# Kernel optimization log

Measured on AMD Instinct MI355X. Metric: run time of the kernel, lower is better.

Reference implementation:

```python
import jax, jax.numpy as jnp
import numpy as np

B, T, H, W, C = 2, 8, 20, 36, 512
NH = 4
HD = C // NH
WS = (5, 9)
EXP = (2, 4)              # window_size // 2
KP = (5, 9)               # focal unfold kernel for level k=0
PADP = (2, 4)
T2T_K, T2T_S, T2T_P = (7, 7), (3, 3), (3, 3)
FFN_HD = 1960
NWH, NWW = H // WS[0], W // WS[1]   # 4, 4
WAREA = WS[0] * WS[1]               # 45


def _valid_ind_rolled():
    wh, ww = WS
    eh, ew = EXP
    m = np.ones((4, wh, ww), np.float32)
    m[0, :wh - eh, :ww - ew] = 0   # tl
    m[1, :wh - eh, ew:] = 0        # tr
    m[2, eh:, :ww - ew] = 0        # bl
    m[3, eh:, ew:] = 0             # br
    return jnp.asarray(np.nonzero(m.reshape(-1))[0])

VALID_ROLLED = _valid_ind_rolled()  # (120,)


def unfold(x, k, s, p):
    # x: (N, Cc, Hh, Ww) -> (N, Cc*kh*kw, L); matches torch.nn.Unfold layout (c slowest).
    N, Cc, Hh, Ww = x.shape
    kh, kw = k; sh, sw = s; ph, pw = p
    xp = jnp.pad(x, ((0, 0), (0, 0), (ph, ph), (pw, pw)))
    oh = (Hh + 2 * ph - kh) // sh + 1
    ow = (Ww + 2 * pw - kw) // sw + 1
    cols = [xp[:, :, i:i + oh * sh:sh, j:j + ow * sw:sw]
            for i in range(kh) for j in range(kw)]
    patches = jnp.stack(cols, axis=2)            # (N, Cc, kh*kw, oh, ow)
    return patches.reshape(N, Cc * kh * kw, oh * ow)


def fold(patches, out_hw, k, s, p):
    # inverse of unfold (overlap-add), matches torch F.fold.
    N = patches.shape[0]
    kh, kw = k; sh, sw = s; ph, pw = p
    Hh, Ww = out_hw
    oh = (Hh + 2 * ph - kh) // sh + 1
    ow = (Ww + 2 * pw - kw) // sw + 1
    Cc = patches.shape[1] // (kh * kw)
    pr = patches.reshape(N, Cc, kh, kw, oh, ow)
    out = jnp.zeros((N, Cc, Hh + 2 * ph, Ww + 2 * pw), patches.dtype)
    for i in range(kh):
        for j in range(kw):
            out = out.at[:, :, i:i + oh * sh:sh, j:j + ow * sw:sw].add(pr[:, :, i, j])
    return out[:, :, ph:ph + Hh, pw:pw + Ww]


def layer_norm(x, g, b):
    mu = jnp.mean(x, -1, keepdims=True)
    var = jnp.var(x, -1, keepdims=True)
    return (x - mu) * jax.lax.rsqrt(var + 1e-5) * g + b


def win_part(x):
    # (B,T,H,W,C) -> (B*nW, T*wh*ww, C)
    b = x.shape[0]
    x = x.reshape(b, T, NWH, WS[0], NWW, WS[1], C)
    return x.transpose(0, 2, 4, 1, 3, 5, 6).reshape(-1, T * WAREA, C)


def to_heads(w):
    return w.reshape(-1, T, WAREA, NH, HD).transpose(0, 3, 1, 2, 4).reshape(-1, NH, T * WAREA, HD)


def block_forward(x, g1, be1, wqkv, bqkv, wproj, bproj, wpool, bpool, g2, be2, w1, bf1, w2, bf2, out_h, out_w):
    shortcut = x
    xn = layer_norm(x, g1, be1)

    # ---- coarser (pooled) focal level, k=0 (focal_level=2) ----
    wnr = xn.reshape(B, T, NWH, WS[0], NWW, WS[1], C).transpose(0, 2, 4, 1, 3, 5, 6)
    wnr = wnr.reshape(B, NWH, NWW, T, WAREA, C)
    pooled = jnp.einsum('bhwtnc,n->bhwtc', wnr, wpool) + bpool   # (B,NWH,NWW,T,C)

    # ---- window attention ----
    qkv = xn @ wqkv + bqkv                                       # (B,T,H,W,3C)
    q, k, v = jnp.split(qkv, 3, axis=-1)
    qw = to_heads(win_part(q)) * (HD ** -0.5)
    kw_, vw = to_heads(win_part(k)), to_heads(win_part(v))

    def rolled(t):
        parts = []
        for sh, sw in ((-EXP[0], -EXP[1]), (-EXP[0], EXP[1]), (EXP[0], -EXP[1]), (EXP[0], EXP[1])):
            r = jnp.roll(t, (sh, sw), axis=(2, 3))
            parts.append(win_part(r).reshape(-1, T, WAREA, NH, HD))
        cat = jnp.concatenate(parts, axis=2)                     # (B*nW, T, 4*warea, NH, HD)
        cat = jnp.take(cat.transpose(0, 3, 1, 2, 4), VALID_ROLLED, axis=3)
        return cat.reshape(-1, NH, T * VALID_ROLLED.shape[0], HD)

    k_rolled = jnp.concatenate([kw_, rolled(k)], axis=2)         # (B*nW, NH, T*165, HD)
    v_rolled = jnp.concatenate([vw, rolled(v)], axis=2)

    # pooled keys/values via focal unfold
    xp = pooled.transpose(0, 3, 1, 2, 4)                          # (B,T,NWH,NWW,C)
    qkv_p = xp @ wqkv + bqkv
    kp, vp = qkv_p[..., C:2 * C], qkv_p[..., 2 * C:]

    def unfold_kv(t):
        t = t.transpose(0, 1, 4, 2, 3).reshape(B * T, C, NWH, NWW)
        u = unfold(t, KP, (1, 1), PADP)                           # (B*T, C*45, L)
        L = u.shape[-1]
        u = u.reshape(B, T, C, KP[0], KP[1], L).transpose(0, 5, 1, 3, 4, 2)
        u = u.reshape(B * L, T, KP[0] * KP[1], NH, HD).transpose(0, 3, 1, 2, 4)
        return u.reshape(B * L, NH, T * KP[0] * KP[1], HD)

    k_all = jnp.concatenate([k_rolled, unfold_kv(kp)], axis=2)
    v_all = jnp.concatenate([v_rolled, unfold_kv(vp)], axis=2)

    attn = jnp.einsum('wnqd,wnkd->wnqk', qw, k_all)               # (B*nW, NH, T*45, N)

    # validity mask for pooled context (zero-padded unfold positions -> -100)
    ones = jnp.ones((T, 1, NWH, NWW), x.dtype)
    um = unfold(ones, KP, (1, 1), PADP)                           # (T, 45, L)
    L = um.shape[-1]
    mvals = jnp.where(um.reshape(T, KP[0] * KP[1], L).transpose(2, 0, 1).reshape(L, -1) == 0,
                      jnp.asarray(-100.0, x.dtype), jnp.asarray(0.0, x.dtype))
    n_rolled = k_rolled.shape[2]
    mask_cols = jnp.concatenate([jnp.zeros((L, n_rolled), x.dtype), mvals], axis=1)
    attn = attn + jnp.tile(mask_cols, (B, 1))[:, None, None, :]

    attn = jax.nn.softmax(attn, axis=-1)
    out = jnp.einsum('wnqk,wnkd->wnqd', attn, v_all)
    out = out.transpose(0, 2, 1, 3).reshape(-1, T * WAREA, C) @ wproj + bproj

    # window reverse + residual
    out = out.reshape(B, NWH, NWW, T, WS[0], WS[1], C)
    out = out.transpose(0, 3, 1, 4, 2, 5, 6).reshape(B, T, H, W, C)
    x = shortcut + out

    # ---- FusionFeedForward (fold/unfold re-normalized MLP) ----
    y = layer_norm(x, g2, be2).reshape(B, T * H * W, C)
    h = y @ w1 + bf1                                              # (B, n, 1960)
    nvec = ((out_h + 2 * T2T_P[0] - T2T_K[0]) // T2T_S[0] + 1) * \
           ((out_w + 2 * T2T_P[1] - T2T_K[1]) // T2T_S[1] + 1)
    bt = (B * T * H * W) // nvec
    norm_p = jnp.ones((bt, T2T_K[0] * T2T_K[1], nvec), x.dtype)
    norm_f = fold(norm_p, (out_h, out_w), T2T_K, T2T_S, T2T_P)    # (bt,1,out_h,out_w)
    h_f = fold(h.reshape(bt, nvec, FFN_HD).transpose(0, 2, 1), (out_h, out_w), T2T_K, T2T_S, T2T_P)
    h = unfold(h_f / norm_f, T2T_K, T2T_S, T2T_P).transpose(0, 2, 1).reshape(B, T * H * W, FFN_HD)
    h = jax.nn.gelu(h, approximate=False) @ w2 + bf2
    return x + h.reshape(B, T, H, W, C)


def setup_inputs() -> dict:
    key = jax.random.key(0)
    ks = jax.random.split(key, 8)
    s = 0.02
    return dict(
        x=jax.random.normal(ks[0], (B, T, H, W, C), jnp.float32),
        g1=jnp.ones((C,), jnp.float32),
        be1=jnp.zeros((C,), jnp.float32),
        wqkv=jax.random.normal(ks[1], (C, 3 * C), jnp.float32) * s,
        bqkv=jnp.zeros((3 * C,), jnp.float32),
        wproj=jax.random.normal(ks[2], (C, C), jnp.float32) * s,
        bproj=jnp.zeros((C,), jnp.float32),
        wpool=jnp.full((WAREA,), 1.0 / WAREA, jnp.float32),
        bpool=jnp.zeros((1,), jnp.float32),
        g2=jnp.ones((C,), jnp.float32),
        be2=jnp.zeros((C,), jnp.float32),
        w1=jax.random.normal(ks[3], (C, FFN_HD), jnp.float32) * s,
        bf1=jnp.zeros((FFN_HD,), jnp.float32),
        w2=jax.random.normal(ks[4], (FFN_HD, C), jnp.float32) * s,
        bf2=jnp.zeros((C,), jnp.float32),
        out_h=60,
        out_w=108,
    )


def reference(x, g1, be1, wqkv, bqkv, wproj, bproj, wpool, bpool, g2, be2, w1, bf1, w2, bf2, out_h, out_w):
    return block_forward(x, g1, be1, wqkv, bqkv, wproj, bproj, wpool, bpool,
                         g2, be2, w1, bf1, w2, bf2, out_h, out_w)
```

## Files before the change

kernel.cpp:

```cpp
#include <hip/hip_runtime.h>
#include <hip/hip_bf16.h>
#include <math.h>

typedef __hip_bfloat16 bf16;
typedef __attribute__((ext_vector_type(8))) short bf16x8;
typedef __attribute__((ext_vector_type(4))) float f32x4;

#define DEVI __device__ __forceinline__

#define C_ 512
#define NH_ 4
#define NTOK 11520
#define NKEY 1680
#define NRK 120
#define FFN_ 1960
#define POOLED_FLAG 0x40000000

DEVI float bfu(unsigned u) { return __uint_as_float(u << 16); }
DEVI void stw(bf16* p, float v) { *p = __float2bfloat16(v); }
DEVI unsigned short f2bs(float f) { bf16 h = __float2bfloat16(f); return *(unsigned short*)&h; }
DEVI unsigned pk2(float a, float b) {
  return (unsigned)f2bs(a) | ((unsigned)f2bs(b) << 16);
}
DEVI float ldwr(const void* p, size_t i, int dt) {
  return dt ? ((const float*)p)[i] : __bfloat162float(((const bf16*)p)[i]);
}

DEVI void gload_lds16(const void* g, void* l) {
  __builtin_amdgcn_global_load_lds(
      (const __attribute__((address_space(1))) void*)g,
      (__attribute__((address_space(3))) void*)l, 16, 0, 0);
}

__global__ void k_detect(const void* __restrict__ g1, int* __restrict__ flag) {
  if (threadIdx.x == 0) {
    const unsigned short* p = (const unsigned short*)g1;
    *flag = (p[0] == 0x3F80u) ? 0 : 1;
  }
}

__global__ void k_prep(int* __restrict__ table) {
  if (threadIdx.x == 0) {
    int cnt = 0;
    for (int p = 0; p < 4; p++)
      for (int wi = 0; wi < 5; wi++)
        for (int wj = 0; wj < 9; wj++) {
          bool invalid;
          if (p == 0)      invalid = (wi < 3) && (wj < 5);
          else if (p == 1) invalid = (wi < 3) && (wj >= 4);
          else if (p == 2) invalid = (wi >= 2) && (wj < 5);
          else             invalid = (wi >= 2) && (wj >= 4);
          if (!invalid) table[cnt++] = p * 45 + wi * 9 + wj;
        }
  }
}

__global__ void k_ksrc(const int* __restrict__ vtab, int* __restrict__ ksrc) {
  int idx = blockIdx.x * 256 + threadIdx.x;
  if (idx >= 32 * NKEY) return;
  int w = idx / NKEY, j = idx % NKEY;
  int b = w >> 4, nh = (w >> 2) & 3, nw = w & 3;
  int val;
  if (j < 360) {
    int t = j / 45, pos = j % 45, wi = pos / 9, wj2 = pos % 9;
    val = ((b * 8 + t) * 20 + nh * 5 + wi) * 36 + nw * 9 + wj2;
  } else if (j < 1320) {
    int jj = j - 360;
    int t = jj / 120, r = jj % 120;
    int id = vtab[r];
    int p = id / 45, pos = id % 45, wi = pos / 9, wj2 = pos % 9;
    int sh = (p < 2) ? -2 : 2;
    int sw = (p & 1) ? 4 : -4;
    int hh = nh * 5 + wi - sh;
    if (hh < 0) hh += 20; else if (hh >= 20) hh -= 20;
    int ww2 = nw * 9 + wj2 - sw;
    if (ww2 < 0) ww2 += 36; else if (ww2 >= 36) ww2 -= 36;
    val = ((b * 8 + t) * 20 + hh) * 36 + ww2;
  } else {
    int jj = j - 1320;
    int t = jj / 45, kidx = jj % 45, ki = kidx / 9, kj = kidx % 9;
    int snh = nh + ki - 2, snw = nw + kj - 4;
    if (snh < 0 || snh >= 4 || snw < 0 || snw >= 4) val = -1;
    else val = POOLED_FLAG | ((b * 8 + t) * 16 + snh * 4 + snw);
  }
  ksrc[idx] = val;
}

__global__ void k_wcvt_all(const int* __restrict__ dflag,
                           const void* __restrict__ w0, const void* __restrict__ w1i,
                           const void* __restrict__ w2i, const void* __restrict__ w3i,
                           bf16* __restrict__ o0, bf16* __restrict__ o1,
                           bf16* __restrict__ o2, bf16* __restrict__ o3) {
  __shared__ unsigned short tile[64][65];
  const int dt = *dflag;
  int bid = blockIdx.x;
  const void* in; bf16* out; int K, N, nn;
  if (bid < 192)      { in = w0;  out = o0; K = 512;  N = 1536; nn = 24; }
  else if (bid < 256) { in = w1i; out = o1; K = 512;  N = 512;  nn = 8;  bid -= 192; }
  else if (bid < 512) { in = w2i; out = o2; K = 512;  N = 1960; nn = 32; bid -= 256; }
  else                { in = w3i; out = o3; K = 1960; N = 512;  nn = 8;  bid -= 512; }
  int tn = bid % nn, tk = bid / nn;
  int n0 = tn * 64, k0 = tk * 64;
  int cr = threadIdx.x >> 6;
  int cc = threadIdx.x & 63;
#pragma unroll
  for (int p = 0; p < 16; p++) {
    int kr = p * 4 + cr;
    float v = 0.f;
    if (k0 + kr < K && n0 + cc < N)
      v = ldwr(in, (size_t)(k0 + kr) * N + n0 + cc, dt);
    tile[kr][cc] = f2bs(v);
  }
  __syncthreads();
#pragma unroll
  for (int p = 0; p < 16; p++) {
    int nr = p * 4 + cr;
    int k = k0 + cc;
    if (k < K) {
      unsigned short u = tile[cc][nr];
      out[(size_t)(n0 + nr) * K + k] = *(bf16*)&u;
    }
  }
}

__global__ void k_bcvt_all(const int* __restrict__ dflag,
                           const void* __restrict__ b0, const void* __restrict__ b1,
                           const void* __restrict__ b2, const void* __restrict__ b3,
                           float* __restrict__ o0, float* __restrict__ o1,
                           float* __restrict__ o2, float* __restrict__ o3) {
  const int dt = *dflag;
  int i = blockIdx.x * 256 + threadIdx.x;
  if (i < 1536)      o0[i] = ldwr(b0, i, dt);
  else if (i < 2048) o1[i - 1536] = ldwr(b1, i - 1536, dt);
  else if (i < 4008) o2[i - 2048] = ldwr(b2, i - 2048, dt);
  else if (i < 4520) o3[i - 4008] = ldwr(b3, i - 4008, dt);
}

__global__ void k_ln(const int* __restrict__ dflag, int xmode,
                     const void* __restrict__ xin, const void* __restrict__ g,
                     const void* __restrict__ be, bf16* __restrict__ out) {
  const int dt = *dflag;
  const int xf32 = xmode | dt;
  const int tok = blockIdx.x;
  const int tid = threadIdx.x;
  const size_t base = (size_t)tok * C_;
  float v0 = ldwr(xin, base + tid, xf32);
  float v1 = ldwr(xin, base + tid + 256, xf32);
  float s = v0 + v1, ss = v0 * v0 + v1 * v1;
#pragma unroll
  for (int o = 32; o; o >>= 1) { s += __shfl_xor(s, o); ss += __shfl_xor(ss, o); }
  __shared__ float sh[10];
  const int lane = tid & 63, wv = tid >> 6;
  if (lane == 0) { sh[wv] = s; sh[4 + wv] = ss; }
  __syncthreads();
  if (tid == 0) {
    float a = sh[0] + sh[1] + sh[2] + sh[3];
    float q = sh[4] + sh[5] + sh[6] + sh[7];
    float mu = a * (1.0f / C_);
    float var = q * (1.0f / C_) - mu * mu;
    sh[8] = mu; sh[9] = rsqrtf(fmaxf(var, 0.f) + 1e-5f);
  }
  __syncthreads();
  float mu = sh[8], inv = sh[9];
  stw(out + base + tid,
      (v0 - mu) * inv * ldwr(g, tid, dt) + ldwr(be, tid, dt));
  stw(out + base + tid + 256,
      (v1 - mu) * inv * ldwr(g, tid + 256, dt) + ldwr(be, tid + 256, dt));
}

__global__ void k_pool(const int* __restrict__ dflag, const bf16* __restrict__ xn,
                       const void* __restrict__ wpool, const void* __restrict__ bpool,
                       float* __restrict__ pooled) {
  const int dt = *dflag;
  int idx = blockIdx.x * blockDim.x + threadIdx.x;
  if (idx >= 256 * C_) return;
  int c = idx & (C_ - 1);
  int fw = idx >> 9;
  int nw = fw & 3, nh = (fw >> 2) & 3;
  int bt = fw >> 4;
  float acc = ldwr(bpool, 0, dt);
  for (int wi = 0; wi < 5; wi++) {
    int hh = nh * 5 + wi;
    const bf16* base = xn + (((size_t)(bt * 20 + hh)) * 36 + nw * 9) * C_ + c;
    for (int wj = 0; wj < 9; wj++)
      acc += __bfloat162float(base[(size_t)wj * C_]) * ldwr(wpool, wi * 9 + wj, dt);
  }
  pooled[idx] = acc;
}

__global__ void k_gemm_small(const int* __restrict__ dflag, const float* __restrict__ A,
                             const void* __restrict__ Bw, const void* __restrict__ bias,
                             float* __restrict__ Cc) {
  const int dt = *dflag;
  int n = blockIdx.x * blockDim.x + threadIdx.x;
  int m = blockIdx.y;
  if (n >= 1536) return;
  float acc = ldwr(bias, n, dt);
  const float* a = A + (size_t)m * C_;
  for (int k = 0; k < C_; k++)
    acc += a[k] * ldwr(Bw, (size_t)k * 1536 + n, dt);
  Cc[(size_t)m * 1536 + n] = acc;
}

DEVI void gemm_store(int dt, int resmode, int outmode, const void* resid, void* out,
                     size_t off, float v) {
  if (resmode)
    v += ((resmode == 2) || dt) ? ((const float*)resid)[off]
                                : __bfloat162float(((const bf16*)resid)[off]);
  if ((outmode == 1) || (outmode == 2 && dt)) ((float*)out)[off] = v;
  else ((bf16*)out)[off] = __float2bfloat16(v);
}

__global__ __launch_bounds__(256) void k_gemm_m(const int* __restrict__ dflag,
                                                int resmode, int outmode,
                                                const bf16* __restrict__ A,
                                                const bf16* __restrict__ Bt,
                                                const float* __restrict__ bias,
                                                const void* __restrict__ resid,
                                                void* __restrict__ out,
                                                int M, int N, int K) {
  const int dt = *dflag;
  __shared__ __align__(16) unsigned short As[128 * 32];
  __shared__ __align__(16) unsigned short Bs[128 * 32];
  const int tid = threadIdx.x;
  const int lane = tid & 63, wid = tid >> 6;
  const int r15 = lane & 15, quad = lane >> 4;
  const int wm = wid >> 1, wn = wid & 1;
  const int m0 = blockIdx.y * 128, n0 = blockIdx.x * 128;

  f32x4 acc[4][4];
#pragma unroll
  for (int i = 0; i < 4; i++)
#pragma unroll
    for (int j = 0; j < 4; j++)
#pragma unroll
      for (int e = 0; e < 4; e++) acc[i][j][e] = 0.f;

  const int lrow = lane >> 2, lcol = (lane & 3) * 8;

  for (int k0 = 0; k0 < K; k0 += 32) {
    int rem = K - k0;
    if (rem >= 32) {
      const bf16* ga = A + (size_t)(m0 + wid * 32 + lrow) * K + k0 + lcol;
      gload_lds16(ga, &As[wid * 1024]);
      gload_lds16(ga + (size_t)16 * K, &As[wid * 1024 + 512]);
      const bf16* gb = Bt + (size_t)(n0 + wid * 32 + lrow) * K + k0 + lcol;
      gload_lds16(gb, &Bs[wid * 1024]);
      gload_lds16(gb + (size_t)16 * K, &Bs[wid * 1024 + 512]);
    } else {
      int r = tid >> 2, c = (tid & 3) * 8;
      uint4 z = make_uint4(0, 0, 0, 0);
      uint4 a0 = z, a1 = z, b0 = z, b1 = z;
      if (c < rem) {
        a0 = *(const uint4*)(A + (size_t)(m0 + r) * K + k0 + c);
        a1 = *(const uint4*)(A + (size_t)(m0 + r + 64) * K + k0 + c);
        b0 = *(const uint4*)(Bt + (size_t)(n0 + r) * K + k0 + c);
        b1 = *(const uint4*)(Bt + (size_t)(n0 + r + 64) * K + k0 + c);
      }
      *(uint4*)&As[r * 32 + c] = a0;
      *(uint4*)&As[(r + 64) * 32 + c] = a1;
      *(uint4*)&Bs[r * 32 + c] = b0;
      *(uint4*)&Bs[(r + 64) * 32 + c] = b1;
    }
    __syncthreads();

    bf16x8 af[4], bfr[4];
#pragma unroll
    for (int mf = 0; mf < 4; mf++)
      af[mf] = *(const bf16x8*)&As[(wm * 64 + mf * 16 + r15) * 32 + quad * 8];
#pragma unroll
    for (int nf = 0; nf < 4; nf++)
      bfr[nf] = *(const bf16x8*)&Bs[(wn * 64 + nf * 16 + r15) * 32 + quad * 8];
#pragma unroll
    for (int mf = 0; mf < 4; mf++)
#pragma unroll
      for (int nf = 0; nf < 4; nf++)
        acc[mf][nf] = __builtin_amdgcn_mfma_f32_16x16x32_bf16(af[mf], bfr[nf],
                                                              acc[mf][nf], 0, 0, 0);
    __syncthreads();
  }

#pragma unroll
  for (int nf = 0; nf < 4; nf++) {
    int n = n0 + wn * 64 + nf * 16 + r15;
    if (n >= N) continue;
    float bv = bias[n];
#pragma unroll
    for (int mf = 0; mf < 4; mf++) {
      int mb = m0 + wm * 64 + mf * 16 + quad * 4;
#pragma unroll
      for (int e = 0; e < 4; e++) {
        size_t off = (size_t)(mb + e) * N + n;
        gemm_store(dt, resmode, outmode, resid, out, off, acc[mf][nf][e] + bv);
      }
    }
  }
}

__global__ __launch_bounds__(256) void k_gemm_s64(const int* __restrict__ dflag,
                                                  int resmode, int outmode,
                                                  const bf16* __restrict__ A,
                                                  const bf16* __restrict__ Bt,
                                                  const float* __restrict__ bias,
                                                  const void* __restrict__ resid,
                                                  void* __restrict__ out,
                                                  int M, int N, int K) {
  const int dt = *dflag;
  __shared__ __align__(16) unsigned short As[64 * 32];
  __shared__ __align__(16) unsigned short Bs[64 * 32];
  const int tid = threadIdx.x;
  const int lane = tid & 63, wid = tid >> 6;
  const int r15 = lane & 15, quad = lane >> 4;
  const int wm = wid >> 1, wn = wid & 1;
  const int m0 = blockIdx.y * 64, n0 = blockIdx.x * 64;

  f32x4 acc[2][2];
#pragma unroll
  for (int i = 0; i < 2; i++)
#pragma unroll
    for (int j = 0; j < 2; j++)
#pragma unroll
      for (int e = 0; e < 4; e++) acc[i][j][e] = 0.f;

  const int lrow = lane >> 2, lcol = (lane & 3) * 8;

  for (int k0 = 0; k0 < K; k0 += 32) {
    int rem = K - k0;
    if (rem >= 32) {
      const bf16* ga = A + (size_t)(m0 + wid * 16 + lrow) * K + k0 + lcol;
      gload_lds16(ga, &As[wid * 512]);
      const bf16* gb = Bt + (size_t)(n0 + wid * 16 + lrow) * K + k0 + lcol;
      gload_lds16(gb, &Bs[wid * 512]);
    } else {
      int r = tid >> 2, c = (tid & 3) * 8;
      uint4 z = make_uint4(0, 0, 0, 0);
      uint4 a0 = z, b0 = z;
      if (c < rem) {
        a0 = *(const uint4*)(A + (size_t)(m0 + r) * K + k0 + c);
        b0 = *(const uint4*)(Bt + (size_t)(n0 + r) * K + k0 + c);
      }
      *(uint4*)&As[r * 32 + c] = a0;
      *(uint4*)&Bs[r * 32 + c] = b0;
    }
    __syncthreads();

    bf16x8 af[2], bfr[2];
#pragma unroll
    for (int mf = 0; mf < 2; mf++)
      af[mf] = *(const bf16x8*)&As[(wm * 32 + mf * 16 + r15) * 32 + quad * 8];
#pragma unroll
    for (int nf = 0; nf < 2; nf++)
      bfr[nf] = *(const bf16x8*)&Bs[(wn * 32 + nf * 16 + r15) * 32 + quad * 8];
#pragma unroll
    for (int mf = 0; mf < 2; mf++)
#pragma unroll
      for (int nf = 0; nf < 2; nf++)
        acc[mf][nf] = __builtin_amdgcn_mfma_f32_16x16x32_bf16(af[mf], bfr[nf],
                                                              acc[mf][nf], 0, 0, 0);
    __syncthreads();
  }

#pragma unroll
  for (int nf = 0; nf < 2; nf++) {
    int n = n0 + wn * 32 + nf * 16 + r15;
    if (n >= N) continue;
    float bv = bias[n];
#pragma unroll
    for (int mf = 0; mf < 2; mf++) {
      int mb = m0 + wm * 32 + mf * 16 + quad * 4;
#pragma unroll
      for (int e = 0; e < 4; e++) {
        size_t off = (size_t)(mb + e) * N + n;
        gemm_store(dt, resmode, outmode, resid, out, off, acc[mf][nf][e] + bv);
      }
    }
  }
}

#define KT 64
#define KPAD 136
#define VPAD 72
__global__ __launch_bounds__(256) void k_attn_m(const bf16* __restrict__ qkv,
                                                const float* __restrict__ qkvp,
                                                const int* __restrict__ ksrc,
                                                bf16* __restrict__ ao) {
  __shared__ int ks_l[NKEY];
  __shared__ __align__(16) unsigned short ktl[KT * KPAD];
  __shared__ __align__(16) unsigned short vtl[128 * VPAD];
  __shared__ __align__(16) unsigned short ptl[4 * 16 * VPAD];
  __shared__ float maskv[KT];

  const int tid = threadIdx.x;
  const int lane = tid & 63, wid = tid >> 6;
  const int r15 = lane & 15, quad = lane >> 4;
  const int w = blockIdx.x, qt = blockIdx.y, n = blockIdx.z;
  const int b = w >> 4, nh = (w >> 2) & 3, nw = w & 3;
  const unsigned short* qkvs = (const unsigned short*)qkv;

  for (int j = tid; j < NKEY; j += 256) ks_l[j] = ksrc[w * NKEY + j];

  bf16x8 qf[4];
  {
    int qw = qt * 64 + wid * 16 + r15;
    int qc2 = qw < 360 ? qw : 359;
    int t = qc2 / 45, pos = qc2 % 45, wi = pos / 9, wj = pos % 9;
    int tok = ((b * 8 + t) * 20 + nh * 5 + wi) * 36 + nw * 9 + wj;
    const unsigned short* qp = qkvs + (size_t)tok * 1536 + n * 128 + quad * 8;
#pragma unroll
    for (int c = 0; c < 4; c++)
      qf[c] = *(const bf16x8*)(qp + c * 32);
  }

  f32x4 of[8];
#pragma unroll
  for (int nt = 0; nt < 8; nt++)
#pragma unroll
    for (int e = 0; e < 4; e++) of[nt][e] = 0.f;
  float m_[4], l_[4];
#pragma unroll
  for (int e = 0; e < 4; e++) { m_[e] = -1e30f; l_[e] = 0.f; }

  unsigned short* ptw = &ptl[wid * 16 * VPAD];
  __syncthreads();

  const int kr = tid >> 2, kp = tid & 3;
  const int vr = lane, vp = wid;
  uint4 kreg[4], vreg[4];
  float mreg = -30000.f;

  auto load_tile = [&](int j0) {
    int cnt = NKEY - j0; if (cnt > KT) cnt = KT;
    {
      int s0 = (kr < cnt) ? ks_l[j0 + kr] : -1;
      mreg = (s0 < 0) ? -30000.f : 0.f;
      if (s0 < 0) {
        kreg[0] = kreg[1] = kreg[2] = kreg[3] = make_uint4(0, 0, 0, 0);
      } else if (s0 & POOLED_FLAG) {
        const float* kf = qkvp + (size_t)(s0 & 0x3FFFFFFF) * 1536 + 512 + n * 128 + kp * 32;
#pragma unroll
        for (int i = 0; i < 4; i++) {
          float4 f0 = ((const float4*)kf)[2 * i], f1 = ((const float4*)kf)[2 * i + 1];
          kreg[i] = make_uint4(pk2(f0.x, f0.y), pk2(f0.z, f0.w),
                               pk2(f1.x, f1.y), pk2(f1.z, f1.w));
        }
      } else {
        const uint4* kq = (const uint4*)(qkvs + (size_t)s0 * 1536 + 512 + n * 128 + kp * 32);
#pragma unroll
        for (int i = 0; i < 4; i++) kreg[i] = kq[i];
      }
    }
    {
      int s1 = (vr < cnt) ? ks_l[j0 + vr] : -1;
      if (s1 < 0) {
        vreg[0] = vreg[1] = vreg[2] = vreg[3] = make_uint4(0, 0, 0, 0);
      } else if (s1 & POOLED_FLAG) {
        const float* vf = qkvp + (size_t)(s1 & 0x3FFFFFFF) * 1536 + 1024 + n * 128 + vp * 32;
#pragma unroll
        for (int i = 0; i < 4; i++) {
          float4 f0 = ((const float4*)vf)[2 * i], f1 = ((const float4*)vf)[2 * i + 1];
          vreg[i] = make_uint4(pk2(f0.x, f0.y), pk2(f0.z, f0.w),
                               pk2(f1.x, f1.y), pk2(f1.z, f1.w));
        }
      } else {
        const uint4* vq = (const uint4*)(qkvs + (size_t)s1 * 1536 + 1024 + n * 128 + vp * 32);
#pragma unroll
        for (int i = 0; i < 4; i++) vreg[i] = vq[i];
      }
    }
  };

  auto store_tile = [&]() {
    if (kp == 0) maskv[kr] = mreg;
#pragma unroll
    for (int i = 0; i < 4; i++)
      *(uint4*)&ktl[kr * KPAD + kp * 32 + i * 8] = kreg[i];
#pragma unroll
    for (int i = 0; i < 4; i++) {
      uint4 u = vreg[i];
      int d0 = vp * 32 + i * 8;
      vtl[(d0 + 0) * VPAD + vr] = (unsigned short)(u.x & 0xFFFFu);
      vtl[(d0 + 1) * VPAD + vr] = (unsigned short)(u.x >> 16);
      vtl[(d0 + 2) * VPAD + vr] = (unsigned short)(u.y & 0xFFFFu);
      vtl[(d0 + 3) * VPAD + vr] = (unsigned short)(u.y >> 16);
      vtl[(d0 + 4) * VPAD + vr] = (unsigned short)(u.z & 0xFFFFu);
      vtl[(d0 + 5) * VPAD + vr] = (unsigned short)(u.z >> 16);
      vtl[(d0 + 6) * VPAD + vr] = (unsigned short)(u.w & 0xFFFFu);
      vtl[(d0 + 7) * VPAD + vr] = (unsigned short)(u.w >> 16);
    }
  };

  load_tile(0);
  store_tile();
  __syncthreads();

  int j0 = 0;
  while (true) {
    int nxt = j0 + KT;
    if (nxt < NKEY) load_tile(nxt);

    f32x4 sf[4];
#pragma unroll
    for (int ft = 0; ft < 4; ft++)
#pragma unroll
      for (int e = 0; e < 4; e++) sf[ft][e] = 0.f;
#pragma unroll
    for (int kc = 0; kc < 4; kc++) {
      bf16x8 a = qf[kc];
#pragma unroll
      for (int ft = 0; ft < 4; ft++) {
        bf16x8 bb = *(const bf16x8*)&ktl[(ft * 16 + r15) * KPAD + kc * 32 + quad * 8];
        sf[ft] = __builtin_amdgcn_mfma_f32_16x16x32_bf16(a, bb, sf[ft], 0, 0, 0);
      }
    }
    const float scl = 0.088388347648318447f;
#pragma unroll
    for (int ft = 0; ft < 4; ft++) {
      float mk = maskv[ft * 16 + r15];
#pragma unroll
      for (int e = 0; e < 4; e++) sf[ft][e] = sf[ft][e] * scl + mk;
    }
    float tm[4], rs[4];
#pragma unroll
    for (int e = 0; e < 4; e++) {
      float v = fmaxf(fmaxf(sf[0][e], sf[1][e]), fmaxf(sf[2][e], sf[3][e]));
#pragma unroll
      for (int o = 1; o < 16; o <<= 1) v = fmaxf(v, __shfl_xor(v, o));
      tm[e] = v;
    }
#pragma unroll
    for (int e = 0; e < 4; e++) {
      float mn = fmaxf(m_[e], tm[e]);
      float alpha = __expf(m_[e] - mn);
      m_[e] = mn;
      rs[e] = 0.f;
#pragma unroll
      for (int ft = 0; ft < 4; ft++) {
        float pv = __expf(sf[ft][e] - mn);
        rs[e] += pv;
        ptw[(quad * 4 + e) * VPAD + ft * 16 + r15] = f2bs(pv);
      }
#pragma unroll
      for (int o = 1; o < 16; o <<= 1) rs[e] += __shfl_xor(rs[e], o);
      l_[e] = l_[e] * alpha + rs[e];
#pragma unroll
      for (int nt = 0; nt < 8; nt++) of[nt][e] *= alpha;
    }
#pragma unroll
    for (int kc = 0; kc < 2; kc++) {
      bf16x8 pa = *(const bf16x8*)&ptw[r15 * VPAD + kc * 32 + quad * 8];
#pragma unroll
      for (int nt = 0; nt < 8; nt++) {
        bf16x8 vb = *(const bf16x8*)&vtl[(nt * 16 + r15) * VPAD + kc * 32 + quad * 8];
        of[nt] = __builtin_amdgcn_mfma_f32_16x16x32_bf16(pa, vb, of[nt], 0, 0, 0);
      }
    }

    if (nxt >= NKEY) break;
    __syncthreads();
    store_tile();
    __syncthreads();
    j0 = nxt;
  }

#pragma unroll
  for (int e = 0; e < 4; e++) {
    int qw = qt * 64 + wid * 16 + quad * 4 + e;
    if (qw >= 360) continue;
    float inv = 1.0f / l_[e];
    int t = qw / 45, pos = qw % 45, wi = pos / 9, wj = pos % 9;
    int tok = ((b * 8 + t) * 20 + nh * 5 + wi) * 36 + nw * 9 + wj;
    bf16* op = ao + (size_t)tok * 512 + n * 128 + r15;
#pragma unroll
    for (int nt = 0; nt < 8; nt++)
      stw(op + nt * 16, of[nt][e] * inv);
  }
}

__global__ void k_fold(const bf16* __restrict__ h1, float* __restrict__ hf) {
  int idx = blockIdx.x * 256 + threadIdx.x;
  if (idx >= 16 * 40 * 60 * 108) return;
  int x = idx % 108;
  int tmp = idx / 108;
  int y = tmp % 60; tmp /= 60;
  int c = tmp % 40;
  int bt = tmp / 40;
  float sum = 0.f;
  int cnt = 0;
  for (int ki = y % 3; ki < 7; ki += 3) {
    int num = y + 3 - ki;
    if (num < 0) continue;
    int oh = num / 3;
    if (oh >= 20) continue;
    for (int kj = x % 3; kj < 7; kj += 3) {
      int num2 = x + 3 - kj;
      if (num2 < 0) continue;
      int ow = num2 / 3;
      if (ow >= 36) continue;
      sum += __bfloat162float(
          h1[(size_t)(bt * 720 + oh * 36 + ow) * FFN_ + c * 49 + ki * 7 + kj]);
      cnt++;
    }
  }
  hf[idx] = sum / (float)cnt;
}

__global__ void k_unfold_gelu(const float* __restrict__ hf, bf16* __restrict__ h2) {
  int idx = blockIdx.x * 256 + threadIdx.x;
  if (idx >= NTOK * FFN_) return;
  int f = idx % FFN_;
  int token = idx / FFN_;
  int c = f / 49, k = f % 49, ki = k / 7, kj = k % 7;
  int bt = token / 720, vec = token % 720;
  int oh = vec / 36, ow = vec % 36;
  int y = oh * 3 + ki - 3, x = ow * 3 + kj - 3;
  float v = 0.f;
  if (y >= 0 && y < 60 && x >= 0 && x < 108)
    v = hf[((size_t)(bt * 40 + c) * 60 + y) * 108 + x];
  float g = 0.5f * v * (1.0f + erff(v * 0.70710678118654752f));
  stw(h2 + idx, g);
}

extern "C" void kernel_launch(void* const* d_in, const int* in_sizes, int n_in,
                              void* d_out, int out_size, void* d_ws, size_t ws_size,
                              hipStream_t stream) {
  (void)in_sizes; (void)n_in; (void)out_size; (void)ws_size;
  const void* x     = d_in[0];
  const void* g1    = d_in[1];
  const void* be1   = d_in[2];
  const void* wqkv  = d_in[3];
  const void* bqkv  = d_in[4];
  const void* wproj = d_in[5];
  const void* bproj = d_in[6];
  const void* wpool = d_in[7];
  const void* bpool = d_in[8];
  const void* g2    = d_in[9];
  const void* be2   = d_in[10];
  const void* w1    = d_in[11];
  const void* bf1   = d_in[12];
  const void* w2    = d_in[13];
  const void* bf2   = d_in[14];

  char* ws = (char*)d_ws;
  size_t off = 0;
  auto alloc = [&](size_t bytes) -> void* {
    void* p = ws + off;
    off += (bytes + 255) & ~(size_t)255;
    return p;
  };

  int*   dflag  = (int*)  alloc(256);
  int*   vtab   = (int*)  alloc(NRK * sizeof(int));
  int*   ksrc   = (int*)  alloc((size_t)32 * NKEY * sizeof(int));
  bf16*  buf2   = (bf16*) alloc((size_t)NTOK * FFN_ * 2);
  float* pooled = (float*)alloc((size_t)256 * C_ * 4);
  float* qkvp   = (float*)alloc((size_t)256 * 1536 * 4);
  float* x2     = (float*)alloc((size_t)NTOK * C_ * 4);
  float* hf     = (float*)alloc((size_t)16 * 40 * 60 * 108 * 4);
  bf16*  wqkv_t = (bf16*) alloc((size_t)1536 * 512 * 2);
  bf16*  wproj_t= (bf16*) alloc((size_t)512 * 512 * 2);
  bf16*  w1_t   = (bf16*) alloc((size_t)2048 * 512 * 2);
  bf16*  w2_t   = (bf16*) alloc((size_t)512 * FFN_ * 2);
  float* bqkv_f = (float*)alloc(1536 * 4);
  float* bproj_f= (float*)alloc(512 * 4);
  float* bf1_f  = (float*)alloc(FFN_ * 4);
  float* bf2_f  = (float*)alloc(512 * 4);

  bf16* buf1 = (bf16*)d_out;
  bf16* xn = buf1;
  bf16* ao = buf1;
  bf16* y  = buf1;
  bf16* qkv = buf2;
  bf16* h1  = buf2;

  k_detect<<<1, 64, 0, stream>>>(g1, dflag);
  k_prep<<<1, 64, 0, stream>>>(vtab);
  k_ksrc<<<(32 * NKEY) / 256, 256, 0, stream>>>(vtab, ksrc);

  k_wcvt_all<<<760, 256, 0, stream>>>(dflag, wqkv, wproj, w1, w2,
                                      wqkv_t, wproj_t, w1_t, w2_t);
  k_bcvt_all<<<18, 256, 0, stream>>>(dflag, bqkv, bproj, bf1, bf2,
                                     bqkv_f, bproj_f, bf1_f, bf2_f);

  k_ln<<<NTOK, 256, 0, stream>>>(dflag, 0, x, g1, be1, xn);

  k_pool<<<512, 256, 0, stream>>>(dflag, xn, wpool, bpool, pooled);

  k_gemm_m<<<dim3(12, 90), 256, 0, stream>>>(
      dflag, 0, 0, xn, wqkv_t, bqkv_f, nullptr, qkv, NTOK, 1536, 512);

  k_gemm_small<<<dim3(6, 256), 256, 0, stream>>>(dflag, pooled, wqkv, bqkv, qkvp);

  k_attn_m<<<dim3(32, 6, NH_), 256, 0, stream>>>(qkv, qkvp, ksrc, ao);

  k_gemm_s64<<<dim3(8, 180), 256, 0, stream>>>(
      dflag, 1, 1, ao, wproj_t, bproj_f, x, x2, NTOK, 512, 512);

  k_ln<<<NTOK, 256, 0, stream>>>(dflag, 1, x2, g2, be2, y);

  k_gemm_m<<<dim3(16, 90), 256, 0, stream>>>(
      dflag, 0, 0, y, w1_t, bf1_f, nullptr, h1, NTOK, FFN_, 512);

  k_fold<<<(16 * 40 * 60 * 108) / 256, 256, 0, stream>>>(h1, hf);

  k_unfold_gelu<<<(NTOK * FFN_) / 256, 256, 0, stream>>>(hf, h1);

  k_gemm_s64<<<dim3(8, 180), 256, 0, stream>>>(
      dflag, 2, 2, h1, w2_t, bf2_f, x2, d_out, NTOK, 512, FFN_);
}
```

Before: 654.2 us.

## Emit transposed FFN1 output for coalesced fold; unify GEMMs on 128-tile kernel

The first FFN GEMM now runs with its operands swapped, so it writes h1 transposed (feature-major, token-contiguous). The fold kernel's gathers then read contiguous tokens instead of striding by FFN width, and a per-row bias mode plus zero-padded bias to 2048 rows support this. The 64x64 GEMM kernel is removed, and the projection and FFN2 GEMMs now use the 128x128 MFMA kernel. That raises per-block reuse but launches fewer blocks (360) and relies on that kernel handling K=1960 tails correctly.

```diff
diff --git a/kernel.cpp b/kernel.cpp
--- a/kernel.cpp
+++ b/kernel.cpp
@@ -132,8 +132,8 @@
   int i = blockIdx.x * 256 + threadIdx.x;
   if (i < 1536)      o0[i] = ldwr(b0, i, dt);
   else if (i < 2048) o1[i - 1536] = ldwr(b1, i - 1536, dt);
-  else if (i < 4008) o2[i - 2048] = ldwr(b2, i - 2048, dt);
-  else if (i < 4520) o3[i - 4008] = ldwr(b3, i - 4008, dt);
+  else if (i < 4096) { int j = i - 2048; o2[j] = (j < FFN_) ? ldwr(b2, j, dt) : 0.f; }
+  else if (i < 4608) o3[i - 4096] = ldwr(b3, i - 4096, dt);
 }
 
 __global__ void k_ln(const int* __restrict__ dflag, int xmode,
@@ -212,7 +212,7 @@
 }
 
 __global__ __launch_bounds__(256) void k_gemm_m(const int* __restrict__ dflag,
-                                                int resmode, int outmode,
+                                                int resmode, int outmode, int biasmode,
                                                 const bf16* __restrict__ A,
                                                 const bf16* __restrict__ Bt,
                                                 const float* __restrict__ bias,
@@ -284,93 +284,14 @@
   for (int nf = 0; nf < 4; nf++) {
     int n = n0 + wn * 64 + nf * 16 + r15;
     if (n >= N) continue;
-    float bv = bias[n];
+    float bvc = biasmode ? 0.f : bias[n];
 #pragma unroll
     for (int mf = 0; mf < 4; mf++) {
       int mb = m0 + wm * 64 + mf * 16 + quad * 4;
 #pragma unroll
       for (int e = 0; e < 4; e++) {
         size_t off = (size_t)(mb + e) * N + n;
-        gemm_store(dt, resmode, outmode, resid, out, off, acc[mf][nf][e] + bv);
-      }
-    }
-  }
-}
-
-__global__ __launch_bounds__(256) void k_gemm_s64(const int* __restrict__ dflag,
-                                                  int resmode, int outmode,
-                                                  const bf16* __restrict__ A,
-                                                  const bf16* __restrict__ Bt,
-                                                  const float* __restrict__ bias,
-                                                  const void* __restrict__ resid,
-                                                  void* __restrict__ out,
-                                                  int M, int N, int K) {
-  const int dt = *dflag;
-  __shared__ __align__(16) unsigned short As[64 * 32];
-  __shared__ __align__(16) unsigned short Bs[64 * 32];
-  const int tid = threadIdx.x;
-  const int lane = tid & 63, wid = tid >> 6;
-  const int r15 = lane & 15, quad = lane >> 4;
-  const int wm = wid >> 1, wn = wid & 1;
-  const int m0 = blockIdx.y * 64, n0 = blockIdx.x * 64;
-
-  f32x4 acc[2][2];
-#pragma unroll
-  for (int i = 0; i < 2; i++)
-#pragma unroll
-    for (int j = 0; j < 2; j++)
-#pragma unroll
-      for (int e = 0; e < 4; e++) acc[i][j][e] = 0.f;
-
-  const int lrow = lane >> 2, lcol = (lane & 3) * 8;
-
-  for (int k0 = 0; k0 < K; k0 += 32) {
-    int rem = K - k0;
-    if (rem >= 32) {
-      const bf16* ga = A + (size_t)(m0 + wid * 16 + lrow) * K + k0 + lcol;
-      gload_lds16(ga, &As[wid * 512]);
-      const bf16* gb = Bt + (size_t)(n0 + wid * 16 + lrow) * K + k0 + lcol;
-      gload_lds16(gb, &Bs[wid * 512]);
-    } else {
-      int r = tid >> 2, c = (tid & 3) * 8;
-      uint4 z = make_uint4(0, 0, 0, 0);
-      uint4 a0 = z, b0 = z;
-      if (c < rem) {
-        a0 = *(const uint4*)(A + (size_t)(m0 + r) * K + k0 + c);
-        b0 = *(const uint4*)(Bt + (size_t)(n0 + r) * K + k0 + c);
-      }
-      *(uint4*)&As[r * 32 + c] = a0;
-      *(uint4*)&Bs[r * 32 + c] = b0;
-    }
-    __syncthreads();
-
-    bf16x8 af[2], bfr[2];
-#pragma unroll
-    for (int mf = 0; mf < 2; mf++)
-      af[mf] = *(const bf16x8*)&As[(wm * 32 + mf * 16 + r15) * 32 + quad * 8];
-#pragma unroll
-    for (int nf = 0; nf < 2; nf++)
-      bfr[nf] = *(const bf16x8*)&Bs[(wn * 32 + nf * 16 + r15) * 32 + quad * 8];
-#pragma unroll
-    for (int mf = 0; mf < 2; mf++)
-#pragma unroll
-      for (int nf = 0; nf < 2; nf++)
-        acc[mf][nf] = __builtin_amdgcn_mfma_f32_16x16x32_bf16(af[mf], bfr[nf],
-                                                              acc[mf][nf], 0, 0, 0);
-    __syncthreads();
-  }
-
-#pragma unroll
-  for (int nf = 0; nf < 2; nf++) {
-    int n = n0 + wn * 32 + nf * 16 + r15;
-    if (n >= N) continue;
-    float bv = bias[n];
-#pragma unroll
-    for (int mf = 0; mf < 2; mf++) {
-      int mb = m0 + wm * 32 + mf * 16 + quad * 4;
-#pragma unroll
-      for (int e = 0; e < 4; e++) {
-        size_t off = (size_t)(mb + e) * N + n;
+        float bv = biasmode ? bias[mb + e] : bvc;
         gemm_store(dt, resmode, outmode, resid, out, off, acc[mf][nf][e] + bv);
       }
     }
@@ -576,7 +497,7 @@
   }
 }
 
-__global__ void k_fold(const bf16* __restrict__ h1, float* __restrict__ hf) {
+__global__ void k_fold(const bf16* __restrict__ h1T, float* __restrict__ hf) {
   int idx = blockIdx.x * 256 + threadIdx.x;
   if (idx >= 16 * 40 * 60 * 108) return;
   int x = idx % 108;
@@ -597,7 +518,7 @@
       int ow = num2 / 3;
       if (ow >= 36) continue;
       sum += __bfloat162float(
-          h1[(size_t)(bt * 720 + oh * 36 + ow) * FFN_ + c * 49 + ki * 7 + kj]);
+          h1T[(size_t)(c * 49 + ki * 7 + kj) * NTOK + bt * 720 + oh * 36 + ow]);
       cnt++;
     }
   }
@@ -651,7 +572,7 @@
   int*   dflag  = (int*)  alloc(256);
   int*   vtab   = (int*)  alloc(NRK * sizeof(int));
   int*   ksrc   = (int*)  alloc((size_t)32 * NKEY * sizeof(int));
-  bf16*  buf2   = (bf16*) alloc((size_t)NTOK * FFN_ * 2);
+  bf16*  buf2   = (bf16*) alloc((size_t)2048 * NTOK * 2);
   float* pooled = (float*)alloc((size_t)256 * C_ * 4);
   float* qkvp   = (float*)alloc((size_t)256 * 1536 * 4);
   float* x2     = (float*)alloc((size_t)NTOK * C_ * 4);
@@ -662,7 +583,7 @@
   bf16*  w2_t   = (bf16*) alloc((size_t)512 * FFN_ * 2);
   float* bqkv_f = (float*)alloc(1536 * 4);
   float* bproj_f= (float*)alloc(512 * 4);
-  float* bf1_f  = (float*)alloc(FFN_ * 4);
+  float* bf1_f  = (float*)alloc(2048 * 4);
   float* bf2_f  = (float*)alloc(512 * 4);
 
   bf16* buf1 = (bf16*)d_out;
@@ -670,7 +591,8 @@
   bf16* ao = buf1;
   bf16* y  = buf1;
   bf16* qkv = buf2;
-  bf16* h1  = buf2;
+  bf16* h1T = buf2;
+  bf16* h2  = buf2;
 
   k_detect<<<1, 64, 0, stream>>>(g1, dflag);
   k_prep<<<1, 64, 0, stream>>>(vtab);
@@ -686,24 +608,24 @@
   k_pool<<<512, 256, 0, stream>>>(dflag, xn, wpool, bpool, pooled);
 
   k_gemm_m<<<dim3(12, 90), 256, 0, stream>>>(
-      dflag, 0, 0, xn, wqkv_t, bqkv_f, nullptr, qkv, NTOK, 1536, 512);
+      dflag, 0, 0, 0, xn, wqkv_t, bqkv_f, nullptr, qkv, NTOK, 1536, 512);
 
   k_gemm_small<<<dim3(6, 256), 256, 0, stream>>>(dflag, pooled, wqkv, bqkv, qkvp);
 
   k_attn_m<<<dim3(32, 6, NH_), 256, 0, stream>>>(qkv, qkvp, ksrc, ao);
 
-  k_gemm_s64<<<dim3(8, 180), 256, 0, stream>>>(
-      dflag, 1, 1, ao, wproj_t, bproj_f, x, x2, NTOK, 512, 512);
+  k_gemm_m<<<dim3(4, 90), 256, 0, stream>>>(
+      dflag, 1, 1, 0, ao, wproj_t, bproj_f, x, x2, NTOK, 512, 512);
 
   k_ln<<<NTOK, 256, 0, stream>>>(dflag, 1, x2, g2, be2, y);
 
-  k_gemm_m<<<dim3(16, 90), 256, 0, stream>>>(
-      dflag, 0, 0, y, w1_t, bf1_f, nullptr, h1, NTOK, FFN_, 512);
-
-  k_fold<<<(16 * 40 * 60 * 108) / 256, 256, 0, stream>>>(h1, hf);
-
-  k_unfold_gelu<<<(NTOK * FFN_) / 256, 256, 0, stream>>>(hf, h1);
-
-  k_gemm_s64<<<dim3(8, 180), 256, 0, stream>>>(
-      dflag, 2, 2, h1, w2_t, bf2_f, x2, d_out, NTOK, 512, FFN_);
-}
+  k_gemm_m<<<dim3(90, 16), 256, 0, stream>>>(
+      dflag, 0, 0, 1, w1_t, y, bf1_f, nullptr, h1T, 2048, NTOK, 512);
+
+  k_fold<<<(16 * 40 * 60 * 108) / 256, 256, 0, stream>>>(h1T, hf);
+
+  k_unfold_gelu<<<(NTOK * FFN_) / 256, 256, 0, stream>>>(hf, h2);
+
+  k_gemm_m<<<dim3(4, 90), 256, 0, stream>>>(
+      dflag, 2, 2, 0, h2, w2_t, bf2_f, x2, d_out, NTOK, 512, 1960);
+}
```

Result: slower. 684.7 us (+4.7%).
